# Kernel tuning notes

Hardware: AMD Instinct MI355X
Metric: run time of the kernel (lower is better)

The kernel has to match this reference:

```python
import jax, jax.numpy as jnp
import numpy as np

N = 50000      # nodes
E2 = 400000    # undirected edges
E = 2 * E2     # directed edges (each undirected edge in both directions)
DIN = 512      # input feature dim
DH = 128       # MLP hidden
C = 8          # num classes / BP channels


def setup_inputs() -> dict:
    key = jax.random.key(0)
    ks = jax.random.split(key, 9)
    x = jax.random.normal(ks[0], (N, DIN), jnp.float32)
    src0 = jax.random.randint(ks[1], (E2,), 0, N)
    dst0 = jax.random.randint(ks[2], (E2,), 0, N)
    # symmetric directed edge list: row 0 = source j, row 1 = target i
    edge_index = jnp.stack([jnp.concatenate([src0, dst0]),
                            jnp.concatenate([dst0, src0])])
    w0 = jax.random.uniform(ks[3], (E2,), jnp.float32, 0.5, 1.5)
    edge_weight = jnp.concatenate([w0, w0])  # reverse edge shares weight
    # edge_rv[e] = index of the reverse of edge e
    edge_rv = jnp.concatenate([jnp.arange(E2) + E2, jnp.arange(E2)])
    W1 = jax.random.normal(ks[4], (DIN, DH), jnp.float32) * 0.05
    b1 = jnp.zeros((DH,), jnp.float32)
    W2 = jax.random.normal(ks[5], (DH, C), jnp.float32) * 0.05
    b2 = jnp.zeros((C,), jnp.float32)
    param = jax.random.normal(ks[6], (C, C), jnp.float32) * 0.1
    return {"x": x, "edge_index": edge_index, "edge_weight": edge_weight,
            "edge_rv": edge_rv, "W1": W1, "b1": b1, "W2": W2, "b2": b2,
            "param": param, "K": 5}


def log_normalize(log_x):
    return log_x - jax.nn.logsumexp(log_x, axis=-1, keepdims=True)


def reference(x, edge_index, edge_weight, edge_rv, W1, b1, W2, b2, param, K):
    # MLP transform + LogSoftmax -> initial log-beliefs [N, C]
    h = jax.nn.relu(x @ W1 + b1)
    log_b0 = jax.nn.log_softmax(h @ W2 + b2, axis=-1)

    # learn_H=True: logH = logsigmoid(param + param^T), [C, C]
    logH = jax.nn.log_sigmoid(param + param.T)
    src, dst = edge_index[0], edge_index[1]
    # per-edge coupling matrix [E, C, C]
    logC = edge_weight[:, None, None] * logH[None, :, :]

    log_b = log_b0
    log_msg = None
    for _ in range(K):
        x_j = log_b[src]                       # gather source beliefs [E, C]
        if log_msg is not None:
            x_j = x_j - log_msg[edge_rv]       # remove reverse message
        # tropical-semiring matvec in log domain: logsumexp over source channel
        log_msg = log_normalize(jax.nn.logsumexp(x_j[:, :, None] + logC, axis=1))
        agg = jax.ops.segment_sum(log_msg, dst, num_segments=N)  # scatter-add
        log_b = log_normalize(log_b0 + agg)
    return log_b
```

## Files before the change

### kernel.cpp

```cpp
#include <hip/hip_runtime.h>
#include <hip/hip_bf16.h>
#include <hip/hip_fp16.h>
#include <math.h>

#define NN 50000
#define EE 800000
#define E2K 400000
#define DINK 512
#define DHK 128
#define CK 8
#define KIT 5
#define NBLKS 196
#define EPT 4

typedef __attribute__((ext_vector_type(8))) short short8;
typedef __attribute__((ext_vector_type(4))) float f32x4;

__device__ __forceinline__ unsigned short f2bf(float f) {
    union { float f; unsigned int u; } v;
    v.f = f;
    unsigned int u = v.u;
    unsigned int r = (u + 0x7FFFu + ((u >> 16) & 1u)) >> 16;
    return (unsigned short)r;
}
__device__ __forceinline__ float bfu2f(unsigned int lo16) {
    union { unsigned int u; float f; } v;
    v.u = lo16 << 16;
    return v.f;
}

__global__ __launch_bounds__(256) void prep_kernel(
    const float* __restrict__ W1, const float* __restrict__ param,
    unsigned short* __restrict__ W1t, float* __restrict__ logH,
    int* __restrict__ cnt) {
    if (blockIdx.x < 256) {
        int idx = blockIdx.x * 256 + threadIdx.x;
        int n = idx >> 9;
        int k = idx & 511;
        W1t[idx] = f2bf(W1[(size_t)k * DHK + n]);
    } else if (blockIdx.x == 256) {
        if (threadIdx.x < 64) {
            int t = threadIdx.x;
            int i = t >> 3, j = t & 7;
            float z = param[i * 8 + j] + param[j * 8 + i];
            logH[t] = fminf(z, 0.0f) - log1pf(expf(-fabsf(z)));
        }
    } else {
        int i = (blockIdx.x - 257) * 256 + threadIdx.x;
        if (i < NN) cnt[i] = 0;
    }
}

__device__ __forceinline__ void mlp_load(const float* const* xptr,
                                         const unsigned short* const* bptr,
                                         int koff, float4 (&ar)[4][2],
                                         short8 (&bc)[4]) {
#pragma unroll
    for (int mt = 0; mt < 4; ++mt) {
        ar[mt][0] = *(const float4*)(xptr[mt] + koff);
        ar[mt][1] = *(const float4*)(xptr[mt] + koff + 4);
    }
#pragma unroll
    for (int nt = 0; nt < 4; ++nt) bc[nt] = *(const short8*)(bptr[nt] + koff);
}

__device__ __forceinline__ void mlp_step(const float4 (&ar)[4][2],
                                         const short8 (&bc)[4],
                                         f32x4 (&acc)[4][4]) {
    short8 af[4];
#pragma unroll
    for (int mt = 0; mt < 4; ++mt) {
        union { short8 s; __hip_bfloat162 h[4]; } cv;
        cv.h[0] = __float22bfloat162_rn(make_float2(ar[mt][0].x, ar[mt][0].y));
        cv.h[1] = __float22bfloat162_rn(make_float2(ar[mt][0].z, ar[mt][0].w));
        cv.h[2] = __float22bfloat162_rn(make_float2(ar[mt][1].x, ar[mt][1].y));
        cv.h[3] = __float22bfloat162_rn(make_float2(ar[mt][1].z, ar[mt][1].w));
        af[mt] = cv.s;
    }
#pragma unroll
    for (int mt = 0; mt < 4; ++mt)
#pragma unroll
        for (int nt = 0; nt < 4; ++nt)
            acc[mt][nt] = __builtin_amdgcn_mfma_f32_16x16x32_bf16(
                af[mt], bc[nt], acc[mt][nt], 0, 0, 0);
}

__global__ __launch_bounds__(256) void mlp_mfma_kernel(
    const float* __restrict__ x, const unsigned short* __restrict__ W1t,
    const float* __restrict__ b1, const float* __restrict__ W2,
    const float* __restrict__ b2, float* __restrict__ logb0) {
    __shared__ unsigned short hs[128 * 136];
    __shared__ float W2s[128 * 8];
    __shared__ float b1s[128];
    __shared__ float b2s[8];

    const int tid = threadIdx.x;
    const int wave = tid >> 6;
    const int lane = tid & 63;
    const int q = lane >> 4;
    const int lm = lane & 15;
    const int wm = wave >> 1, wn = wave & 1;
    const int n0 = blockIdx.x * 128;

    if (tid < 128) b1s[tid] = b1[tid];
    if (tid < 8) b2s[tid] = b2[tid];
    {
        int i = tid * 4;
        *(float4*)&W2s[i] = *(const float4*)&W2[i];
    }
    __syncthreads();

    const float* xptr[4];
#pragma unroll
    for (int mt = 0; mt < 4; ++mt) {
        int r = n0 + wm * 64 + mt * 16 + lm;
        if (r > NN - 1) r = NN - 1;
        xptr[mt] = x + (size_t)r * DINK + q * 8;
    }
    const unsigned short* bptr[4];
#pragma unroll
    for (int nt = 0; nt < 4; ++nt) {
        int c = wn * 64 + nt * 16 + lm;
        bptr[nt] = W1t + (size_t)c * DINK + q * 8;
    }

    f32x4 acc[4][4];
#pragma unroll
    for (int mt = 0; mt < 4; ++mt)
#pragma unroll
        for (int nt = 0; nt < 4; ++nt) acc[mt][nt] = (f32x4){0.f, 0.f, 0.f, 0.f};

    float4 arA[4][2], arB[4][2];
    short8 bcA[4], bcB[4];
    mlp_load(xptr, bptr, 0, arA, bcA);
    mlp_load(xptr, bptr, 32, arB, bcB);

#pragma unroll
    for (int k0 = 0; k0 < DINK; k0 += 64) {
        mlp_step(arA, bcA, acc);
        if (k0 + 64 < DINK) mlp_load(xptr, bptr, k0 + 64, arA, bcA);
        mlp_step(arB, bcB, acc);
        if (k0 + 96 < DINK) mlp_load(xptr, bptr, k0 + 96, arB, bcB);
    }

#pragma unroll
    for (int nt = 0; nt < 4; ++nt) {
        int j = wn * 64 + nt * 16 + lm;
        float bj = b1s[j];
#pragma unroll
        for (int mt = 0; mt < 4; ++mt) {
            int rbase = wm * 64 + mt * 16 + q * 4;
#pragma unroll
            for (int r = 0; r < 4; ++r) {
                float h = fmaxf(acc[mt][nt][r] + bj, 0.0f);
                hs[(rbase + r) * 136 + j] = f2bf(h);
            }
        }
    }
    __syncthreads();

    int row = tid >> 1;
    int half = tid & 1;
    const unsigned short* hp = &hs[row * 136 + half * 64];
    float p[8] = {0.f, 0.f, 0.f, 0.f, 0.f, 0.f, 0.f, 0.f};
#pragma unroll
    for (int ch = 0; ch < 8; ++ch) {
        uint4 c4 = *(const uint4*)(hp + ch * 8);
        unsigned int uu[4] = {c4.x, c4.y, c4.z, c4.w};
#pragma unroll
        for (int p2 = 0; p2 < 4; ++p2) {
            float h0 = bfu2f(uu[p2] & 0xFFFFu);
            float h1 = bfu2f(uu[p2] >> 16);
            int j = half * 64 + ch * 8 + p2 * 2;
            const float* w0 = &W2s[j * 8];
            const float* w1 = &W2s[(j + 1) * 8];
#pragma unroll
            for (int c = 0; c < 8; ++c) p[c] = fmaf(h0, w0[c], p[c]);
#pragma unroll
            for (int c = 0; c < 8; ++c) p[c] = fmaf(h1, w1[c], p[c]);
        }
    }
#pragma unroll
    for (int c = 0; c < 8; ++c) p[c] += __shfl_xor(p[c], 1, 64);
    int grow = n0 + row;
    if (half == 0 && grow < NN) {
        float v[8];
        float mx = -1e30f;
#pragma unroll
        for (int c = 0; c < 8; ++c) {
            v[c] = p[c] + b2s[c];
            mx = fmaxf(mx, v[c]);
        }
        float s = 0.0f;
#pragma unroll
        for (int c = 0; c < 8; ++c) s += expf(v[c] - mx);
        float ln = mx + logf(s);
        float4* p0 = (float4*)&logb0[(size_t)grow * 8];
        p0[0] = make_float4(v[0] - ln, v[1] - ln, v[2] - ln, v[3] - ln);
        p0[1] = make_float4(v[4] - ln, v[5] - ln, v[6] - ln, v[7] - ln);
    }
}


__global__ __launch_bounds__(256) void deg_pair_kernel(const int* __restrict__ ei,
                                                       int* __restrict__ cnt) {
    int e = blockIdx.x * 256 + threadIdx.x;
    if (e >= E2K) return;
    int s = ei[e];
    int d = ei[EE + e];
    atomicAdd(&cnt[d], 1);
    atomicAdd(&cnt[s], 1);
}

__global__ __launch_bounds__(256) void scan_partial_kernel(
    const int* __restrict__ cnt, int* __restrict__ partial) {
    __shared__ int sd[256];
    int t = threadIdx.x;
    int i = blockIdx.x * 256 + t;
    sd[t] = (i < NN) ? cnt[i] : 0;
    __syncthreads();
#pragma unroll
    for (int s = 128; s > 0; s >>= 1) {
        if (t < s) sd[t] += sd[t + s];
        __syncthreads();
    }
    if (t == 0) partial[blockIdx.x] = sd[0];
}

__global__ __launch_bounds__(256) void scan_write2_kernel(
    const int* __restrict__ cnt, const int* __restrict__ partial,
    int* __restrict__ off, int* __restrict__ cnt_z) {
    __shared__ int sd[256];
    const int t = threadIdx.x;
    const int b = blockIdx.x;
    sd[t] = (t < NBLKS) ? partial[t] : 0;
    __syncthreads();
#pragma unroll
    for (int s = 1; s < 256; s <<= 1) {
        int a = sd[t];
        int v = (t >= s) ? sd[t - s] : 0;
        __syncthreads();
        sd[t] = a + v;
        __syncthreads();
    }
    const int top = (b > 0) ? sd[b - 1] : 0;
    __syncthreads();
    int i = b * 256 + t;
    int v = (i < NN) ? cnt[i] : 0;
    sd[t] = v;
    __syncthreads();
#pragma unroll
    for (int s = 1; s < 256; s <<= 1) {
        int a = sd[t];
        int w = (t >= s) ? sd[t - s] : 0;
        __syncthreads();
        sd[t] = a + w;
        __syncthreads();
    }
    if (i < NN) {
        off[i] = top + sd[t] - v;
        cnt_z[i] = 0;
    }
    if (i == NN - 1) off[NN] = EE;
}

__global__ __launch_bounds__(256) void pos_pair_kernel(
    const int* __restrict__ ei, const float* __restrict__ ew,
    const int* __restrict__ off, int* __restrict__ cnt,
    int2* __restrict__ rw) {
    int e = blockIdx.x * 256 + threadIdx.x;
    if (e >= E2K) return;
    int s = ei[e];
    int d = ei[EE + e];
    int wbits = __float_as_int(ew[e]);
    int pA = off[d] + atomicAdd(&cnt[d], 1);
    int pB = off[s] + atomicAdd(&cnt[s], 1);
    int2 v;
    v.x = pB; v.y = wbits; rw[pA] = v;
    v.x = pA;              rw[pB] = v;
}

__global__ __launch_bounds__(256) void zinit_kernel(
    const float* __restrict__ logb0, const int* __restrict__ off,
    _Float16* __restrict__ z) {
    const int t = threadIdx.x;
    const int n = blockIdx.x * 32 + (t >> 3);
    const int c = t & 7;
    if (n >= NN) return;
    _Float16 v = (_Float16)logb0[(size_t)n * 8 + c];
    const int j0 = off[n];
    const int j1 = off[n + 1];
    for (int j = j0; j < j1; ++j) z[(size_t)j * 8 + c] = v;
}

__global__ __launch_bounds__(256) void msg_kernel(
    const int2* __restrict__ rw, const float* __restrict__ logH,
    const uint4* __restrict__ zbuf, uint4* __restrict__ msg_next) {
    __shared__ float lH[64];
    const int t = threadIdx.x;
    if (t < 64) lH[t] = logH[t];
    __syncthreads();

    const int base = blockIdx.x * (256 * EPT) + t;

    int2 h[EPT];
#pragma unroll
    for (int e = 0; e < EPT; ++e) {
        int j = base + e * 256;
        int jc = (j < EE) ? j : (EE - 1);
        h[e] = rw[jc];
    }
    uint4 zv[EPT];
#pragma unroll
    for (int e = 0; e < EPT; ++e) zv[e] = zbuf[h[e].x];

#pragma unroll
    for (int e = 0; e < EPT; ++e) {
        float w = __int_as_float(h[e].y);
        union { uint4 u; _Float16 hh[8]; } cv;
        cv.u = zv[e];
        float xj[8];
#pragma unroll
        for (int k = 0; k < 8; ++k) xj[k] = (float)cv.hh[k];
        float mg[8];
#pragma unroll
        for (int c2 = 0; c2 < 8; ++c2) {
            float ssum = 0.0f;
#pragma unroll
            for (int c1 = 0; c1 < 8; ++c1)
                ssum += __expf(fmaf(w, lH[c1 * 8 + c2], xj[c1]));
            mg[c2] = __logf(ssum);
        }
        union { uint4 u; _Float16 hh[8]; } ov;
#pragma unroll
        for (int k = 0; k < 8; ++k) ov.hh[k] = (_Float16)mg[k];
        int j = base + e * 256;
        if (j < EE) msg_next[j] = ov.u;
    }
}

__global__ __launch_bounds__(256) void agg_kernel(
    const float* __restrict__ logb0, const int* __restrict__ off,
    const uint4* __restrict__ msg, _Float16* __restrict__ z,
    float* __restrict__ out, int last) {
    const int t = threadIdx.x;
    const int n = blockIdx.x * 32 + (t >> 3);
    const int c = t & 7;
    if (n >= NN) return;
    float a = logb0[(size_t)n * 8 + c];
    const int j0 = off[n];
    const int j1 = off[n + 1];
    const _Float16* mh = (const _Float16*)msg;
    float s0 = 0.f, s1 = 0.f, s2 = 0.f, s3 = 0.f;
    int j = j0;
    for (; j + 4 <= j1; j += 4) {
        s0 += (float)mh[(size_t)(j + 0) * 8 + c];
        s1 += (float)mh[(size_t)(j + 1) * 8 + c];
        s2 += (float)mh[(size_t)(j + 2) * 8 + c];
        s3 += (float)mh[(size_t)(j + 3) * 8 + c];
    }
    for (; j < j1; ++j) s0 += (float)mh[(size_t)j * 8 + c];
    a += (s0 + s1) + (s2 + s3);
    float mx = a;
#pragma unroll
    for (int s = 1; s < 8; s <<= 1) mx = fmaxf(mx, __shfl_xor(mx, s, 8));
    float sum = __expf(a - mx);
#pragma unroll
    for (int s = 1; s < 8; s <<= 1) sum += __shfl_xor(sum, s, 8);
    float v = a - (mx + __logf(sum));
    if (last) {
        out[(size_t)n * 8 + c] = v;
    } else {
        for (int jj = j0; jj < j1; ++jj)
            z[(size_t)jj * 8 + c] = (_Float16)(v - (float)mh[(size_t)jj * 8 + c]);
    }
}

extern "C" void kernel_launch(void* const* d_in, const int* in_sizes, int n_in,
                              void* d_out, int out_size, void* d_ws, size_t ws_size,
                              hipStream_t stream) {
    const float* x = (const float*)d_in[0];
    const int* ei = (const int*)d_in[1];
    const float* ew = (const float*)d_in[2];
    const float* W1 = (const float*)d_in[4];
    const float* b1 = (const float*)d_in[5];
    const float* W2 = (const float*)d_in[6];
    const float* b2 = (const float*)d_in[7];
    const float* param = (const float*)d_in[8];
    float* out = (float*)d_out;

    float* wsf = (float*)d_ws;
    float* logH = wsf;
    float* logb0 = logH + 64;
    uint4* msgbuf = (uint4*)(logb0 + (size_t)NN * 8);
    uint4* zbuf = msgbuf + EE;
    int* off = (int*)(zbuf + EE);
    int2* rw = (int2*)(off + 50004);
    unsigned short* W1t = (unsigned short*)(rw + EE);
    int* cnt = (int*)msgbuf;
    int* partial = cnt + NN;

    const int ZB = (NN + 255) / 256;
    prep_kernel<<<257 + ZB, 256, 0, stream>>>(W1, param, W1t, logH, cnt);
    mlp_mfma_kernel<<<(NN + 127) / 128, 256, 0, stream>>>(x, W1t, b1, W2, b2,
                                                          logb0);

    const int E2B = (E2K + 255) / 256;
    deg_pair_kernel<<<E2B, 256, 0, stream>>>(ei, cnt);
    scan_partial_kernel<<<NBLKS, 256, 0, stream>>>(cnt, partial);
    scan_write2_kernel<<<NBLKS, 256, 0, stream>>>(cnt, partial, off, cnt);
    pos_pair_kernel<<<E2B, 256, 0, stream>>>(ei, ew, off, cnt, rw);

    const int AB = (NN + 31) / 32;
    zinit_kernel<<<AB, 256, 0, stream>>>(logb0, off, (_Float16*)zbuf);

    const int MB = (EE + 256 * EPT - 1) / (256 * EPT);
    for (int it = 0; it < KIT; ++it) {
        msg_kernel<<<MB, 256, 0, stream>>>(rw, logH, zbuf, msgbuf);
        agg_kernel<<<AB, 256, 0, stream>>>(logb0, off, msgbuf,
                                           (_Float16*)zbuf, out,
                                           it == KIT - 1 ? 1 : 0);
    }
}
```

Baseline: 479.4 us.

## Fuse per-iteration message and aggregation kernels into one node-blocked BP kernel

Merges the separate message computation and per-node aggregation kernels into a single kernel that, for each block of 32 destination nodes, computes incoming edge messages into shared memory, reduces them, normalizes, and writes the next iteration's cavity inputs directly. It ping-pongs between two z buffers instead of round-tripping messages through global memory. It also folds the edge-position kernel and z initialization into one launch. The aim is to drop the global message write and re-read and halve the launch count per iteration. In exchange, blocks with more than CAP edges must recompute messages in a second pass, and per-block work now varies with node degree.

New measurement: 419.8 us. 1.14x faster.

```diff
diff --git a/kernel.cpp b/kernel.cpp
--- a/kernel.cpp
+++ b/kernel.cpp
@@ -11,7 +11,8 @@
 #define CK 8
 #define KIT 5
 #define NBLKS 196
-#define EPT 4
+#define NPB 32
+#define CAP 1024
 
 typedef __attribute__((ext_vector_type(8))) short short8;
 typedef __attribute__((ext_vector_type(4))) float f32x4;
@@ -264,103 +265,101 @@
     if (i == NN - 1) off[NN] = EE;
 }
 
-__global__ __launch_bounds__(256) void pos_pair_kernel(
+__global__ __launch_bounds__(256) void pos_zinit_kernel(
     const int* __restrict__ ei, const float* __restrict__ ew,
     const int* __restrict__ off, int* __restrict__ cnt,
-    int2* __restrict__ rw) {
-    int e = blockIdx.x * 256 + threadIdx.x;
-    if (e >= E2K) return;
-    int s = ei[e];
-    int d = ei[EE + e];
-    int wbits = __float_as_int(ew[e]);
-    int pA = off[d] + atomicAdd(&cnt[d], 1);
-    int pB = off[s] + atomicAdd(&cnt[s], 1);
-    int2 v;
-    v.x = pB; v.y = wbits; rw[pA] = v;
-    v.x = pA;              rw[pB] = v;
-}
-
-__global__ __launch_bounds__(256) void zinit_kernel(
+    int2* __restrict__ rw, const float* __restrict__ logb0,
+    _Float16* __restrict__ z, int E2B) {
+    const int t = threadIdx.x;
+    if ((int)blockIdx.x < E2B) {
+        int e = blockIdx.x * 256 + t;
+        if (e >= E2K) return;
+        int s = ei[e];
+        int d = ei[EE + e];
+        int wbits = __float_as_int(ew[e]);
+        int pA = off[d] + atomicAdd(&cnt[d], 1);
+        int pB = off[s] + atomicAdd(&cnt[s], 1);
+        int2 v;
+        v.x = pB; v.y = wbits; rw[pA] = v;
+        v.x = pA;              rw[pB] = v;
+    } else {
+        int b = blockIdx.x - E2B;
+        int n = b * 32 + (t >> 3);
+        int c = t & 7;
+        if (n >= NN) return;
+        _Float16 v = (_Float16)logb0[(size_t)n * 8 + c];
+        int j0 = off[n];
+        int j1 = off[n + 1];
+        for (int j = j0; j < j1; ++j) z[(size_t)j * 8 + c] = v;
+    }
+}
+
+__global__ __launch_bounds__(256) void bp_fused_kernel(
     const float* __restrict__ logb0, const int* __restrict__ off,
-    _Float16* __restrict__ z) {
-    const int t = threadIdx.x;
-    const int n = blockIdx.x * 32 + (t >> 3);
-    const int c = t & 7;
-    if (n >= NN) return;
-    _Float16 v = (_Float16)logb0[(size_t)n * 8 + c];
-    const int j0 = off[n];
-    const int j1 = off[n + 1];
-    for (int j = j0; j < j1; ++j) z[(size_t)j * 8 + c] = v;
-}
-
-__global__ __launch_bounds__(256) void msg_kernel(
     const int2* __restrict__ rw, const float* __restrict__ logH,
-    const uint4* __restrict__ zbuf, uint4* __restrict__ msg_next) {
+    const uint4* __restrict__ zprev, _Float16* __restrict__ znext,
+    float* __restrict__ out, int last) {
+    __shared__ _Float16 smg[CAP * 8];
+    __shared__ float sb[NPB * 8];
+    __shared__ unsigned char dln[CAP];
     __shared__ float lH[64];
     const int t = threadIdx.x;
     if (t < 64) lH[t] = logH[t];
-    __syncthreads();
-
-    const int base = blockIdx.x * (256 * EPT) + t;
-
-    int2 h[EPT];
-#pragma unroll
-    for (int e = 0; e < EPT; ++e) {
-        int j = base + e * 256;
-        int jc = (j < EE) ? j : (EE - 1);
-        h[e] = rw[jc];
-    }
-    uint4 zv[EPT];
-#pragma unroll
-    for (int e = 0; e < EPT; ++e) zv[e] = zbuf[h[e].x];
-
-#pragma unroll
-    for (int e = 0; e < EPT; ++e) {
-        float w = __int_as_float(h[e].y);
-        union { uint4 u; _Float16 hh[8]; } cv;
-        cv.u = zv[e];
-        float xj[8];
-#pragma unroll
-        for (int k = 0; k < 8; ++k) xj[k] = (float)cv.hh[k];
-        float mg[8];
-#pragma unroll
-        for (int c2 = 0; c2 < 8; ++c2) {
-            float ssum = 0.0f;
-#pragma unroll
-            for (int c1 = 0; c1 < 8; ++c1)
-                ssum += __expf(fmaf(w, lH[c1 * 8 + c2], xj[c1]));
-            mg[c2] = __logf(ssum);
-        }
-        union { uint4 u; _Float16 hh[8]; } ov;
-#pragma unroll
-        for (int k = 0; k < 8; ++k) ov.hh[k] = (_Float16)mg[k];
-        int j = base + e * 256;
-        if (j < EE) msg_next[j] = ov.u;
-    }
-}
-
-__global__ __launch_bounds__(256) void agg_kernel(
-    const float* __restrict__ logb0, const int* __restrict__ off,
-    const uint4* __restrict__ msg, _Float16* __restrict__ z,
-    float* __restrict__ out, int last) {
-    const int t = threadIdx.x;
-    const int n = blockIdx.x * 32 + (t >> 3);
+
+    const int n0 = blockIdx.x * NPB;
+    const int nend = (n0 + NPB < NN) ? (n0 + NPB) : NN;
+    const int jb0 = off[n0];
+    const int jb1 = off[nend];
+    const int nl = t >> 3;
     const int c = t & 7;
-    if (n >= NN) return;
-    float a = logb0[(size_t)n * 8 + c];
-    const int j0 = off[n];
-    const int j1 = off[n + 1];
-    const _Float16* mh = (const _Float16*)msg;
-    float s0 = 0.f, s1 = 0.f, s2 = 0.f, s3 = 0.f;
-    int j = j0;
-    for (; j + 4 <= j1; j += 4) {
-        s0 += (float)mh[(size_t)(j + 0) * 8 + c];
-        s1 += (float)mh[(size_t)(j + 1) * 8 + c];
-        s2 += (float)mh[(size_t)(j + 2) * 8 + c];
-        s3 += (float)mh[(size_t)(j + 3) * 8 + c];
-    }
-    for (; j < j1; ++j) s0 += (float)mh[(size_t)j * 8 + c];
-    a += (s0 + s1) + (s2 + s3);
+    const int n = n0 + nl;
+
+    float a = 0.0f;
+    int jn0 = 0, jn1 = 0;
+    if (n < nend) {
+        jn0 = off[n];
+        jn1 = off[n + 1];
+        a = logb0[(size_t)n * 8 + c];
+    }
+    __syncthreads();
+
+    const int single = (jb1 - jb0) <= CAP;
+
+    for (int cb = jb0; cb < jb1; cb += CAP) {
+        int ce = (cb + CAP < jb1) ? (cb + CAP) : jb1;
+        for (int j = cb + t; j < ce; j += 256) {
+            int2 h = rw[j];
+            uint4 zv = zprev[h.x];
+            float w = __int_as_float(h.y);
+            union { uint4 u; _Float16 hh[8]; } cv;
+            cv.u = zv;
+            float xj[8];
+#pragma unroll
+            for (int k = 0; k < 8; ++k) xj[k] = (float)cv.hh[k];
+            float mg[8];
+#pragma unroll
+            for (int c2 = 0; c2 < 8; ++c2) {
+                float ssum = 0.0f;
+#pragma unroll
+                for (int c1 = 0; c1 < 8; ++c1)
+                    ssum += __expf(fmaf(w, lH[c1 * 8 + c2], xj[c1]));
+                mg[c2] = __logf(ssum);
+            }
+            union { uint4 u; _Float16 hh[8]; } ov;
+#pragma unroll
+            for (int k = 0; k < 8; ++k) ov.hh[k] = (_Float16)mg[k];
+            *(uint4*)&smg[(j - cb) * 8] = ov.u;
+        }
+        __syncthreads();
+        int lo = (jn0 > cb) ? jn0 : cb;
+        int hi = (jn1 < ce) ? jn1 : ce;
+        for (int j = lo; j < hi; ++j) {
+            a += (float)smg[(j - cb) * 8 + c];
+            if (c == 0) dln[j - cb] = (unsigned char)nl;
+        }
+        __syncthreads();
+    }
+
     float mx = a;
 #pragma unroll
     for (int s = 1; s < 8; s <<= 1) mx = fmaxf(mx, __shfl_xor(mx, s, 8));
@@ -368,11 +367,55 @@
 #pragma unroll
     for (int s = 1; s < 8; s <<= 1) sum += __shfl_xor(sum, s, 8);
     float v = a - (mx + __logf(sum));
-    if (last) {
-        out[(size_t)n * 8 + c] = v;
-    } else {
-        for (int jj = j0; jj < j1; ++jj)
-            z[(size_t)jj * 8 + c] = (_Float16)(v - (float)mh[(size_t)jj * 8 + c]);
+    if (n < nend) {
+        if (last) out[(size_t)n * 8 + c] = v;
+        sb[nl * 8 + c] = v;
+    }
+    if (last) return;
+    __syncthreads();
+
+    for (int cb = jb0; cb < jb1; cb += CAP) {
+        int ce = (cb + CAP < jb1) ? (cb + CAP) : jb1;
+        if (!single) {
+            for (int j = cb + t; j < ce; j += 256) {
+                int2 h = rw[j];
+                uint4 zv = zprev[h.x];
+                float w = __int_as_float(h.y);
+                union { uint4 u; _Float16 hh[8]; } cv;
+                cv.u = zv;
+                float xj[8];
+#pragma unroll
+                for (int k = 0; k < 8; ++k) xj[k] = (float)cv.hh[k];
+                float mg[8];
+#pragma unroll
+                for (int c2 = 0; c2 < 8; ++c2) {
+                    float ssum = 0.0f;
+#pragma unroll
+                    for (int c1 = 0; c1 < 8; ++c1)
+                        ssum += __expf(fmaf(w, lH[c1 * 8 + c2], xj[c1]));
+                    mg[c2] = __logf(ssum);
+                }
+                union { uint4 u; _Float16 hh[8]; } ov;
+#pragma unroll
+                for (int k = 0; k < 8; ++k) ov.hh[k] = (_Float16)mg[k];
+                *(uint4*)&smg[(j - cb) * 8] = ov.u;
+            }
+            if (c == 0) {
+                int lo = (jn0 > cb) ? jn0 : cb;
+                int hi = (jn1 < ce) ? jn1 : ce;
+                for (int j = lo; j < hi; ++j) dln[j - cb] = (unsigned char)nl;
+            }
+            __syncthreads();
+        }
+        int items = (ce - cb) * 8;
+        for (int item = t; item < items; item += 256) {
+            int jr = item >> 3;
+            int c2 = item & 7;
+            int dl = dln[jr];
+            znext[(size_t)(cb + jr) * 8 + c2] =
+                (_Float16)(sb[dl * 8 + c2] - (float)smg[jr * 8 + c2]);
+        }
+        if (!single) __syncthreads();
     }
 }
 
@@ -392,33 +435,32 @@
     float* wsf = (float*)d_ws;
     float* logH = wsf;
     float* logb0 = logH + 64;
-    uint4* msgbuf = (uint4*)(logb0 + (size_t)NN * 8);
-    uint4* zbuf = msgbuf + EE;
-    int* off = (int*)(zbuf + EE);
+    uint4* zA = (uint4*)(logb0 + (size_t)NN * 8);
+    uint4* zB = zA + EE;
+    int* off = (int*)(zB + EE);
     int2* rw = (int2*)(off + 50004);
     unsigned short* W1t = (unsigned short*)(rw + EE);
-    int* cnt = (int*)msgbuf;
+    int* cnt = (int*)zB;
     int* partial = cnt + NN;
 
-    const int ZB = (NN + 255) / 256;
-    prep_kernel<<<257 + ZB, 256, 0, stream>>>(W1, param, W1t, logH, cnt);
+    const int ZB_ = (NN + 255) / 256;
+    prep_kernel<<<257 + ZB_, 256, 0, stream>>>(W1, param, W1t, logH, cnt);
     mlp_mfma_kernel<<<(NN + 127) / 128, 256, 0, stream>>>(x, W1t, b1, W2, b2,
                                                           logb0);
 
     const int E2B = (E2K + 255) / 256;
+    const int AB = (NN + 31) / 32;
     deg_pair_kernel<<<E2B, 256, 0, stream>>>(ei, cnt);
     scan_partial_kernel<<<NBLKS, 256, 0, stream>>>(cnt, partial);
     scan_write2_kernel<<<NBLKS, 256, 0, stream>>>(cnt, partial, off, cnt);
-    pos_pair_kernel<<<E2B, 256, 0, stream>>>(ei, ew, off, cnt, rw);
-
-    const int AB = (NN + 31) / 32;
-    zinit_kernel<<<AB, 256, 0, stream>>>(logb0, off, (_Float16*)zbuf);
-
-    const int MB = (EE + 256 * EPT - 1) / (256 * EPT);
+    pos_zinit_kernel<<<E2B + AB, 256, 0, stream>>>(ei, ew, off, cnt, rw, logb0,
+                                                   (_Float16*)zA, E2B);
+
+    const int BB = (NN + NPB - 1) / NPB;
+    uint4* zs[2] = {zA, zB};
     for (int it = 0; it < KIT; ++it) {
-        msg_kernel<<<MB, 256, 0, stream>>>(rw, logH, zbuf, msgbuf);
-        agg_kernel<<<AB, 256, 0, stream>>>(logb0, off, msgbuf,
-                                           (_Float16*)zbuf, out,
-                                           it == KIT - 1 ? 1 : 0);
-    }
-}
+        bp_fused_kernel<<<BB, 256, 0, stream>>>(
+            logb0, off, rw, logH, zs[it & 1], (_Float16*)zs[(it + 1) & 1], out,
+            it == KIT - 1 ? 1 : 0);
+    }
+}
```
